# Kernel tuning notes

Measured on AMD Instinct MI355X. Metric: run time of the kernel, lower is better.

The kernel has to match this reference:

```python
import jax, jax.numpy as jnp
import numpy as np

NUM_HEADS = 12
HIDDEN = 768
HEAD = HIDDEN // NUM_HEADS
SCALE = HIDDEN ** (-0.5)  # NB: module scales by hidden_dim**-0.5, not head_size**-0.5


def setup_inputs() -> dict:
    key = jax.random.key(0)
    ks = jax.random.split(key, 8)
    B, N = 16, 512
    std = HIDDEN ** (-0.5)
    return {
        "x": jax.random.normal(ks[0], (B, N, HIDDEN), dtype=jnp.float32),
        "encoding_bias": jax.random.normal(ks[1], (B, N, N), dtype=jnp.float32),
        "Wq": jax.random.normal(ks[2], (HIDDEN, HIDDEN), dtype=jnp.float32) * std,
        "Wk": jax.random.normal(ks[3], (HIDDEN, HIDDEN), dtype=jnp.float32) * std,
        "Wv": jax.random.normal(ks[4], (HIDDEN, HIDDEN), dtype=jnp.float32) * std,
        "bv": jax.random.normal(ks[5], (HIDDEN,), dtype=jnp.float32) * 0.01,
        "Wo": jax.random.normal(ks[6], (HIDDEN, HIDDEN), dtype=jnp.float32) * std,
        "bo": jax.random.normal(ks[7], (HIDDEN,), dtype=jnp.float32) * 0.01,
    }


def reference(x, encoding_bias, Wq, Wk, Wv, bv, Wo, bo):
    B, N, _ = x.shape
    # torch nn.Linear: y = x @ W.T (+ b)
    q = (x @ Wq.T).reshape(B, N, NUM_HEADS, HEAD)
    k = (x @ Wk.T).reshape(B, N, NUM_HEADS, HEAD)
    v = (x @ Wv.T + bv).reshape(B, N, NUM_HEADS, HEAD)
    # scores: [B, H, N, N] with additive graph bias broadcast over heads
    a = jnp.einsum("bnhd,bmhd->bhnm", q, k) * SCALE + encoding_bias[:, None, :, :]
    # data-dependent pad mask: rows whose scores are identically zero
    pad_mask = jnp.all(a == 0, axis=-1)  # [B, H, N]
    a = jnp.where(pad_mask[..., None], -jnp.inf, a)
    a = jax.nn.softmax(a, axis=-1)
    a = jnp.nan_to_num(a)  # all -inf rows -> NaN -> 0
    o = jnp.einsum("bhnm,bmhd->bnhd", a, v).reshape(B, N, HIDDEN)
    # dropout is identity in eval mode
    return o @ Wo.T + bo
```

## Files before the change

kernel.cpp:

```cpp
#include <hip/hip_runtime.h>
#include <stdint.h>

typedef unsigned short u16;
typedef unsigned int u32;
typedef __bf16 bf16x8 __attribute__((ext_vector_type(8)));
typedef float f32x4 __attribute__((ext_vector_type(4)));

#define NH 12
#define HD 64
#define SEQ 512
#define BATCH 16
#define HID 768
#define SCALE_Q 0.03608439182435161f

__device__ __forceinline__ u16 f2bf(float f) {
    u32 u = __builtin_bit_cast(u32, f);
    u32 r = (u + 0x7FFFu + ((u >> 16) & 1u)) >> 16;
    return (u16)r;
}
__device__ __forceinline__ float bf2f(u16 h) {
    return __builtin_bit_cast(float, (u32)h << 16);
}

__device__ __forceinline__ void gl2lds16(const u16* g, u16* lds_base) {
    __builtin_amdgcn_global_load_lds(
        (const __attribute__((address_space(1))) u32*)g,
        (__attribute__((address_space(3))) u32*)lds_base, 16, 0, 0);
}

__global__ void cvt_kernel(const float* __restrict__ src, u16* __restrict__ dst) {
    int i = (blockIdx.x * 256 + threadIdx.x) * 4;
    float4 v = *(const float4*)(src + i);
    ushort4 o;
    o.x = f2bf(v.x); o.y = f2bf(v.y); o.z = f2bf(v.z); o.w = f2bf(v.w);
    *(ushort4*)(dst + i) = o;
}

__global__ void cvt4_kernel(const float* __restrict__ s0, const float* __restrict__ s1,
                            const float* __restrict__ s2, const float* __restrict__ s3,
                            u16* __restrict__ d0, u16* __restrict__ d1,
                            u16* __restrict__ d2, u16* __restrict__ d3) {
    int y = blockIdx.y;
    const float* s = (y == 0) ? s0 : (y == 1) ? s1 : (y == 2) ? s2 : s3;
    u16* d = (y == 0) ? d0 : (y == 1) ? d1 : (y == 2) ? d2 : d3;
    int i = (blockIdx.x * 256 + threadIdx.x) * 4;
    float4 v = *(const float4*)(s + i);
    ushort4 o;
    o.x = f2bf(v.x); o.y = f2bf(v.y); o.z = f2bf(v.z); o.w = f2bf(v.w);
    *(ushort4*)(d + i) = o;
}

__device__ __forceinline__ void gemm_mainloop(
    const u16* __restrict__ Ag, const u16* __restrict__ Bg,
    u16* As, u16* Bs, f32x4 (&acc)[4][4])
{
    const int tid = threadIdx.x;
    const int l = tid & 63, w = tid >> 6;
    const int wm = w & 1, wn = w >> 1;
    const int lr = l & 15, lg = l >> 4;

    const int c0 = tid, c1 = tid + 256;
    const int r0 = c0 >> 2, q0 = (c0 & 3) * 8;
    const int r1 = c1 >> 2, q1 = (c1 & 3) * 8;
    u16* Alds0 = As + w * 512;
    u16* Alds1 = As + 2048 + w * 512;
    u16* Blds0 = Bs + w * 512;
    u16* Blds1 = Bs + 2048 + w * 512;

    for (int k0 = 0; k0 < HID; k0 += 32) {
        __syncthreads();
        gl2lds16(Ag + (size_t)r0 * HID + k0 + q0, Alds0);
        gl2lds16(Ag + (size_t)r1 * HID + k0 + q1, Alds1);
        gl2lds16(Bg + (size_t)r0 * HID + k0 + q0, Blds0);
        gl2lds16(Bg + (size_t)r1 * HID + k0 + q1, Blds1);
        __syncthreads();

        bf16x8 af[4], bfr[4];
#pragma unroll
        for (int mi = 0; mi < 4; mi++)
            af[mi] = *(const bf16x8*)(As + (wm * 64 + mi * 16 + lr) * 32 + lg * 8);
#pragma unroll
        for (int ni = 0; ni < 4; ni++)
            bfr[ni] = *(const bf16x8*)(Bs + (wn * 64 + ni * 16 + lr) * 32 + lg * 8);
#pragma unroll
        for (int mi = 0; mi < 4; mi++)
#pragma unroll
            for (int ni = 0; ni < 4; ni++)
                acc[mi][ni] = __builtin_amdgcn_mfma_f32_16x16x32_bf16(af[mi], bfr[ni], acc[mi][ni], 0, 0, 0);
    }
}

__global__ __launch_bounds__(256, 3) void gemm_qkv(
    const u16* __restrict__ xb, const u16* __restrict__ wq,
    const u16* __restrict__ wk, const u16* __restrict__ wv,
    const float* __restrict__ bv,
    u16* __restrict__ qb, u16* __restrict__ kb, u16* __restrict__ vtb)
{
    __shared__ __align__(16) u16 As[128 * 32];
    __shared__ __align__(16) u16 Bs[128 * 32];
    const int tid = threadIdx.x;
    const int l = tid & 63, w = tid >> 6;
    const int wm = w & 1, wn = w >> 1;
    const int lr = l & 15, lg = l >> 4;
    const int mt = blockIdx.x, nt = blockIdx.y, z = blockIdx.z;

    const u16* Bw = (z == 0) ? wq : (z == 1) ? wk : wv;
    const u16* Ag = xb + (size_t)(mt * 128) * HID;
    const u16* Bg = Bw + (size_t)(nt * 128) * HID;

    f32x4 acc[4][4] = {};
    gemm_mainloop(Ag, Bg, As, Bs, acc);

    const float sc = (z == 0) ? SCALE_Q : 1.0f;
#pragma unroll
    for (int mi = 0; mi < 4; mi++) {
#pragma unroll
        for (int ni = 0; ni < 4; ni++) {
            const int jg = nt * 128 + wn * 64 + ni * 16 + lr;
            const int h = jg >> 6, d = jg & 63;
            if (z < 2) {
                u16* O = (z == 0) ? qb : kb;
#pragma unroll
                for (int r = 0; r < 4; r++) {
                    int ig = mt * 128 + wm * 64 + mi * 16 + lg * 4 + r;
                    int b = ig >> 9, n = ig & 511;
                    O[((size_t)(b * NH + h) * SEQ + n) * HD + d] = f2bf(acc[mi][ni][r] * sc);
                }
            } else {
                float bb = bv[jg];
                int i0 = mt * 128 + wm * 64 + mi * 16 + lg * 4;
                int b = i0 >> 9, m = i0 & 511;
                ushort4 pk;
                pk.x = f2bf(acc[mi][ni][0] + bb);
                pk.y = f2bf(acc[mi][ni][1] + bb);
                pk.z = f2bf(acc[mi][ni][2] + bb);
                pk.w = f2bf(acc[mi][ni][3] + bb);
                *(ushort4*)(vtb + ((size_t)(b * NH + h) * HD + d) * SEQ + m) = pk;
            }
        }
    }
}

__global__ __launch_bounds__(256, 3) void gemm_out(
    const u16* __restrict__ A, const u16* __restrict__ wo,
    const float* __restrict__ bo, float* __restrict__ Cout)
{
    __shared__ __align__(16) u16 As[128 * 32];
    __shared__ __align__(16) u16 Bs[128 * 32];
    const int tid = threadIdx.x;
    const int l = tid & 63, w = tid >> 6;
    const int wm = w & 1, wn = w >> 1;
    const int lr = l & 15, lg = l >> 4;
    const int mt = blockIdx.x, nt = blockIdx.y;

    const u16* Ag = A + (size_t)(mt * 128) * HID;
    const u16* Bg = wo + (size_t)(nt * 128) * HID;

    f32x4 acc[4][4] = {};
    gemm_mainloop(Ag, Bg, As, Bs, acc);

#pragma unroll
    for (int mi = 0; mi < 4; mi++) {
#pragma unroll
        for (int ni = 0; ni < 4; ni++) {
            const int jg = nt * 128 + wn * 64 + ni * 16 + lr;
            float bb = bo[jg];
#pragma unroll
            for (int r = 0; r < 4; r++) {
                int ig = mt * 128 + wm * 64 + mi * 16 + lg * 4 + r;
                Cout[(size_t)ig * HID + jg] = acc[mi][ni][r] + bb;
            }
        }
    }
}

#define LDA 88

__global__ __launch_bounds__(256, 4) void attn_kernel(
    const u16* __restrict__ qb, const u16* __restrict__ kb, const u16* __restrict__ vtb,
    const u16* __restrict__ ebb, u16* __restrict__ ob)
{
    __shared__ __align__(16) u16 Ks[64 * 64];
    __shared__ __align__(16) u16 Vs[64 * 64];
    __shared__ __align__(16) u16 Ps[4][16 * LDA];

    const int tid = threadIdx.x;
    const int l = tid & 63, w = tid >> 6;
    const int lr = l & 15, lg = l >> 4;
    const int qt = blockIdx.x, h = blockIdx.y, b = blockIdx.z;
    const int bh = b * NH + h;
    const int qrow0 = qt * 64 + w * 16;

    const u16* qptr = qb + ((size_t)bh * SEQ + qrow0 + lr) * HD;
    bf16x8 qf0 = *(const bf16x8*)(qptr + lg * 8);
    bf16x8 qf1 = *(const bf16x8*)(qptr + 32 + lg * 8);

    const u16* Kg = kb + (size_t)bh * SEQ * HD;
    const u16* Vg = vtb + (size_t)bh * HD * SEQ;
    const u16* Eg = ebb + ((size_t)b * SEQ + qrow0 + lg * 4) * SEQ;

    f32x4 oacc[4] = {};
    float run_m[4] = {-1e30f, -1e30f, -1e30f, -1e30f};
    float run_l[4] = {0.f, 0.f, 0.f, 0.f};
    int nzf[4] = {0, 0, 0, 0};

    const int p0 = tid, p1 = tid + 256;
    const int kr0 = p0 >> 3, kc0 = (p0 & 7) ^ (kr0 & 7);
    const int kr1 = p1 >> 3, kc1 = (p1 & 7) ^ (kr1 & 7);
    u16* Ks0 = Ks + w * 512;
    u16* Ks1 = Ks + 2048 + w * 512;
    u16* Vs0 = Vs + w * 512;
    u16* Vs1 = Vs + 2048 + w * 512;

    for (int mt0 = 0; mt0 < SEQ; mt0 += 64) {
        u16 bl[4][4];
#pragma unroll
        for (int mi = 0; mi < 4; mi++)
#pragma unroll
            for (int r = 0; r < 4; r++)
                bl[mi][r] = Eg[(size_t)r * SEQ + mt0 + mi * 16 + lr];

        __syncthreads();
        gl2lds16(Kg + (size_t)(mt0 + kr0) * HD + kc0 * 8, Ks0);
        gl2lds16(Kg + (size_t)(mt0 + kr1) * HD + kc1 * 8, Ks1);
        gl2lds16(Vg + (size_t)kr0 * SEQ + mt0 + kc0 * 8, Vs0);
        gl2lds16(Vg + (size_t)kr1 * SEQ + mt0 + kc1 * 8, Vs1);
        __syncthreads();

        float sm[4][4];
#pragma unroll
        for (int mi = 0; mi < 4; mi++) {
            const int row = mi * 16 + lr;
            bf16x8 kf0 = *(const bf16x8*)(Ks + row * 64 + ((lg ^ (row & 7)) * 8));
            bf16x8 kf1 = *(const bf16x8*)(Ks + row * 64 + (((4 + lg) ^ (row & 7)) * 8));
            f32x4 s;
#pragma unroll
            for (int r = 0; r < 4; r++) s[r] = bf2f(bl[mi][r]);
            s = __builtin_amdgcn_mfma_f32_16x16x32_bf16(qf0, kf0, s, 0, 0, 0);
            s = __builtin_amdgcn_mfma_f32_16x16x32_bf16(qf1, kf1, s, 0, 0, 0);
#pragma unroll
            for (int r = 0; r < 4; r++) {
                float sv = s[r];
                nzf[r] |= (sv != 0.0f);
                sm[mi][r] = sv;
            }
        }

        u16* Pw = Ps[w];
#pragma unroll
        for (int r = 0; r < 4; r++) {
            float tm = fmaxf(fmaxf(sm[0][r], sm[1][r]), fmaxf(sm[2][r], sm[3][r]));
            tm = fmaxf(tm, __shfl_xor(tm, 1));
            tm = fmaxf(tm, __shfl_xor(tm, 2));
            tm = fmaxf(tm, __shfl_xor(tm, 4));
            tm = fmaxf(tm, __shfl_xor(tm, 8));
            float nm = fmaxf(run_m[r], tm);
            float alpha = __expf(run_m[r] - nm);
            run_m[r] = nm;
            float ps = 0.f;
#pragma unroll
            for (int mi = 0; mi < 4; mi++) {
                float p = __expf(sm[mi][r] - nm);
                sm[mi][r] = p;
                ps += p;
            }
            ps += __shfl_xor(ps, 1);
            ps += __shfl_xor(ps, 2);
            ps += __shfl_xor(ps, 4);
            ps += __shfl_xor(ps, 8);
            run_l[r] = run_l[r] * alpha + ps;
#pragma unroll
            for (int di = 0; di < 4; di++) oacc[di][r] *= alpha;
        }
#pragma unroll
        for (int mi = 0; mi < 4; mi++)
#pragma unroll
            for (int r = 0; r < 4; r++)
                Pw[(lg * 4 + r) * LDA + mi * 16 + lr] = f2bf(sm[mi][r]);

#pragma unroll
        for (int ks = 0; ks < 2; ks++) {
            bf16x8 pf = *(const bf16x8*)(Pw + lr * LDA + ks * 32 + lg * 8);
#pragma unroll
            for (int di = 0; di < 4; di++) {
                const int row = di * 16 + lr;
                bf16x8 vf = *(const bf16x8*)(Vs + row * 64 + (((ks * 4 + lg) ^ (row & 7)) * 8));
                oacc[di] = __builtin_amdgcn_mfma_f32_16x16x32_bf16(pf, vf, oacc[di], 0, 0, 0);
            }
        }
    }

#pragma unroll
    for (int r = 0; r < 4; r++) {
        int nz = nzf[r];
        nz |= __shfl_xor(nz, 1);
        nz |= __shfl_xor(nz, 2);
        nz |= __shfl_xor(nz, 4);
        nz |= __shfl_xor(nz, 8);
        float inv = nz ? (1.0f / run_l[r]) : 0.0f;
        int n = qrow0 + lg * 4 + r;
        u16* orow = ob + ((size_t)b * SEQ + n) * HID + h * HD;
#pragma unroll
        for (int di = 0; di < 4; di++)
            orow[di * 16 + lr] = f2bf(oacc[di][r] * inv);
    }
}

extern "C" void kernel_launch(void* const* d_in, const int* in_sizes, int n_in,
                              void* d_out, int out_size, void* d_ws, size_t ws_size,
                              hipStream_t stream) {
    (void)in_sizes; (void)n_in; (void)out_size; (void)ws_size;
    const float* x  = (const float*)d_in[0];
    const float* eb = (const float*)d_in[1];
    const float* Wq = (const float*)d_in[2];
    const float* Wk = (const float*)d_in[3];
    const float* Wv = (const float*)d_in[4];
    const float* bv = (const float*)d_in[5];
    const float* Wo = (const float*)d_in[6];
    const float* bo = (const float*)d_in[7];
    float* out = (float*)d_out;

    const int NX = BATCH * SEQ * HID;
    const int NW = HID * HID;
    const int NE = BATCH * SEQ * SEQ;
    u16* ws   = (u16*)d_ws;
    u16* xb   = ws;
    u16* wqb  = xb + NX;
    u16* wkb  = wqb + NW;
    u16* wvb  = wkb + NW;
    u16* wob  = wvb + NW;
    u16* qb   = wob + NW;
    u16* kb   = qb + NX;
    u16* vtb  = kb + NX;
    u16* obuf = vtb + NX;
    u16* ebb  = obuf + NX;

    cvt_kernel<<<NX / 1024, 256, 0, stream>>>(x, xb);
    cvt_kernel<<<NE / 1024, 256, 0, stream>>>(eb, ebb);
    cvt4_kernel<<<dim3(NW / 1024, 4), 256, 0, stream>>>(Wq, Wk, Wv, Wo, wqb, wkb, wvb, wob);

    gemm_qkv<<<dim3(64, 6, 3), 256, 0, stream>>>(xb, wqb, wkb, wvb, bv, qb, kb, vtb);

    attn_kernel<<<dim3(8, NH, BATCH), 256, 0, stream>>>(qb, kb, vtb, ebb, obuf);

    gemm_out<<<dim3(64, 6), 256, 0, stream>>>(obuf, wob, bo, out);
}
```

Before: 220.3 us.

## Double-buffer GEMM and attention LDS tiles, merge conversion kernels, transpose Q store

The GEMM mainloop and the attention K/V loop now use two LDS buffers, prefetching the next tile with global-to-LDS loads while the current one is consumed, and drop one barrier per iteration. The three fp32-to-bf16 conversion launches become a single launch over a contiguous workspace. Q is written transposed with packed 4-element stores, like V, and attention gathers Q with strided scalar loads. Launch bounds change to 4 for the GEMMs and 3 for attention. The larger LDS footprint may reduce occupancy, and the strided Q reads add scattered loads.

```diff
diff --git a/kernel.cpp b/kernel.cpp
--- a/kernel.cpp
+++ b/kernel.cpp
@@ -28,31 +28,41 @@
         (__attribute__((address_space(3))) u32*)lds_base, 16, 0, 0);
 }
 
-__global__ void cvt_kernel(const float* __restrict__ src, u16* __restrict__ dst) {
-    int i = (blockIdx.x * 256 + threadIdx.x) * 4;
-    float4 v = *(const float4*)(src + i);
+#define NXB 6144
+#define NEB 4096
+#define NWB 576
+__global__ void cvt_all(const float* __restrict__ x, const float* __restrict__ eb,
+                        const float* __restrict__ w0, const float* __restrict__ w1,
+                        const float* __restrict__ w2, const float* __restrict__ w3,
+                        u16* __restrict__ dst) {
+    int b = blockIdx.x;
+    const float* s; int sb;
+    if (b < NXB) { s = x; sb = 0; }
+    else if (b < NXB + NEB) { s = eb; sb = NXB; }
+    else if (b < NXB + NEB + NWB) { s = w0; sb = NXB + NEB; }
+    else if (b < NXB + NEB + 2 * NWB) { s = w1; sb = NXB + NEB + NWB; }
+    else if (b < NXB + NEB + 3 * NWB) { s = w2; sb = NXB + NEB + 2 * NWB; }
+    else { s = w3; sb = NXB + NEB + 3 * NWB; }
+    int li = (b - sb) * 1024 + threadIdx.x * 4;
+    float4 v = *(const float4*)(s + li);
     ushort4 o;
     o.x = f2bf(v.x); o.y = f2bf(v.y); o.z = f2bf(v.z); o.w = f2bf(v.w);
-    *(ushort4*)(dst + i) = o;
-}
-
-__global__ void cvt4_kernel(const float* __restrict__ s0, const float* __restrict__ s1,
-                            const float* __restrict__ s2, const float* __restrict__ s3,
-                            u16* __restrict__ d0, u16* __restrict__ d1,
-                            u16* __restrict__ d2, u16* __restrict__ d3) {
-    int y = blockIdx.y;
-    const float* s = (y == 0) ? s0 : (y == 1) ? s1 : (y == 2) ? s2 : s3;
-    u16* d = (y == 0) ? d0 : (y == 1) ? d1 : (y == 2) ? d2 : d3;
-    int i = (blockIdx.x * 256 + threadIdx.x) * 4;
-    float4 v = *(const float4*)(s + i);
-    ushort4 o;
-    o.x = f2bf(v.x); o.y = f2bf(v.y); o.z = f2bf(v.z); o.w = f2bf(v.w);
-    *(ushort4*)(d + i) = o;
+    *(ushort4*)(dst + (size_t)b * 1024 + threadIdx.x * 4) = o;
+}
+
+__device__ __forceinline__ void stage_gemm(
+    const u16* __restrict__ Ag, const u16* __restrict__ Bg, int k0,
+    u16* As, u16* Bs, int r0, int q0, int r1, int q1, int w)
+{
+    gl2lds16(Ag + (size_t)r0 * HID + k0 + q0, As + w * 512);
+    gl2lds16(Ag + (size_t)r1 * HID + k0 + q1, As + 2048 + w * 512);
+    gl2lds16(Bg + (size_t)r0 * HID + k0 + q0, Bs + w * 512);
+    gl2lds16(Bg + (size_t)r1 * HID + k0 + q1, Bs + 2048 + w * 512);
 }
 
 __device__ __forceinline__ void gemm_mainloop(
     const u16* __restrict__ Ag, const u16* __restrict__ Bg,
-    u16* As, u16* Bs, f32x4 (&acc)[4][4])
+    u16 (*As)[128 * 32], u16 (*Bs)[128 * 32], f32x4 (&acc)[4][4])
 {
     const int tid = threadIdx.x;
     const int l = tid & 63, w = tid >> 6;
@@ -62,26 +72,22 @@
     const int c0 = tid, c1 = tid + 256;
     const int r0 = c0 >> 2, q0 = (c0 & 3) * 8;
     const int r1 = c1 >> 2, q1 = (c1 & 3) * 8;
-    u16* Alds0 = As + w * 512;
-    u16* Alds1 = As + 2048 + w * 512;
-    u16* Blds0 = Bs + w * 512;
-    u16* Blds1 = Bs + 2048 + w * 512;
-
-    for (int k0 = 0; k0 < HID; k0 += 32) {
+
+    stage_gemm(Ag, Bg, 0, As[0], Bs[0], r0, q0, r1, q1, w);
+
+    for (int i = 0; i < 24; i++) {
+        const int cur = i & 1;
         __syncthreads();
-        gl2lds16(Ag + (size_t)r0 * HID + k0 + q0, Alds0);
-        gl2lds16(Ag + (size_t)r1 * HID + k0 + q1, Alds1);
-        gl2lds16(Bg + (size_t)r0 * HID + k0 + q0, Blds0);
-        gl2lds16(Bg + (size_t)r1 * HID + k0 + q1, Blds1);
-        __syncthreads();
+        if (i < 23)
+            stage_gemm(Ag, Bg, (i + 1) * 32, As[cur ^ 1], Bs[cur ^ 1], r0, q0, r1, q1, w);
 
         bf16x8 af[4], bfr[4];
 #pragma unroll
         for (int mi = 0; mi < 4; mi++)
-            af[mi] = *(const bf16x8*)(As + (wm * 64 + mi * 16 + lr) * 32 + lg * 8);
+            af[mi] = *(const bf16x8*)(As[cur] + (wm * 64 + mi * 16 + lr) * 32 + lg * 8);
 #pragma unroll
         for (int ni = 0; ni < 4; ni++)
-            bfr[ni] = *(const bf16x8*)(Bs + (wn * 64 + ni * 16 + lr) * 32 + lg * 8);
+            bfr[ni] = *(const bf16x8*)(Bs[cur] + (wn * 64 + ni * 16 + lr) * 32 + lg * 8);
 #pragma unroll
         for (int mi = 0; mi < 4; mi++)
 #pragma unroll
@@ -90,14 +96,14 @@
     }
 }
 
-__global__ __launch_bounds__(256, 3) void gemm_qkv(
+__global__ __launch_bounds__(256, 4) void gemm_qkv(
     const u16* __restrict__ xb, const u16* __restrict__ wq,
     const u16* __restrict__ wk, const u16* __restrict__ wv,
     const float* __restrict__ bv,
-    u16* __restrict__ qb, u16* __restrict__ kb, u16* __restrict__ vtb)
-{
-    __shared__ __align__(16) u16 As[128 * 32];
-    __shared__ __align__(16) u16 Bs[128 * 32];
+    u16* __restrict__ qtb, u16* __restrict__ kb, u16* __restrict__ vtb)
+{
+    __shared__ __align__(16) u16 As[2][128 * 32];
+    __shared__ __align__(16) u16 Bs[2][128 * 32];
     const int tid = threadIdx.x;
     const int l = tid & 63, w = tid >> 6;
     const int wm = w & 1, wn = w >> 1;
@@ -118,35 +124,32 @@
         for (int ni = 0; ni < 4; ni++) {
             const int jg = nt * 128 + wn * 64 + ni * 16 + lr;
             const int h = jg >> 6, d = jg & 63;
-            if (z < 2) {
-                u16* O = (z == 0) ? qb : kb;
-#pragma unroll
-                for (int r = 0; r < 4; r++) {
-                    int ig = mt * 128 + wm * 64 + mi * 16 + lg * 4 + r;
-                    int b = ig >> 9, n = ig & 511;
-                    O[((size_t)(b * NH + h) * SEQ + n) * HD + d] = f2bf(acc[mi][ni][r] * sc);
-                }
+            const int i0 = mt * 128 + wm * 64 + mi * 16 + lg * 4;
+            const int b = i0 >> 9, n0 = i0 & 511;
+            if (z == 1) {
+#pragma unroll
+                for (int r = 0; r < 4; r++)
+                    kb[((size_t)(b * NH + h) * SEQ + n0 + r) * HD + d] = f2bf(acc[mi][ni][r]);
             } else {
-                float bb = bv[jg];
-                int i0 = mt * 128 + wm * 64 + mi * 16 + lg * 4;
-                int b = i0 >> 9, m = i0 & 511;
+                float bb = (z == 2) ? bv[jg] : 0.0f;
                 ushort4 pk;
-                pk.x = f2bf(acc[mi][ni][0] + bb);
-                pk.y = f2bf(acc[mi][ni][1] + bb);
-                pk.z = f2bf(acc[mi][ni][2] + bb);
-                pk.w = f2bf(acc[mi][ni][3] + bb);
-                *(ushort4*)(vtb + ((size_t)(b * NH + h) * HD + d) * SEQ + m) = pk;
-            }
-        }
-    }
-}
-
-__global__ __launch_bounds__(256, 3) void gemm_out(
+                pk.x = f2bf(fmaf(acc[mi][ni][0], sc, bb));
+                pk.y = f2bf(fmaf(acc[mi][ni][1], sc, bb));
+                pk.z = f2bf(fmaf(acc[mi][ni][2], sc, bb));
+                pk.w = f2bf(fmaf(acc[mi][ni][3], sc, bb));
+                u16* O = (z == 0) ? qtb : vtb;
+                *(ushort4*)(O + ((size_t)(b * NH + h) * HD + d) * SEQ + n0) = pk;
+            }
+        }
+    }
+}
+
+__global__ __launch_bounds__(256, 4) void gemm_out(
     const u16* __restrict__ A, const u16* __restrict__ wo,
     const float* __restrict__ bo, float* __restrict__ Cout)
 {
-    __shared__ __align__(16) u16 As[128 * 32];
-    __shared__ __align__(16) u16 Bs[128 * 32];
+    __shared__ __align__(16) u16 As[2][128 * 32];
+    __shared__ __align__(16) u16 Bs[2][128 * 32];
     const int tid = threadIdx.x;
     const int l = tid & 63, w = tid >> 6;
     const int wm = w & 1, wn = w >> 1;
@@ -176,12 +179,22 @@
 
 #define LDA 88
 
-__global__ __launch_bounds__(256, 4) void attn_kernel(
-    const u16* __restrict__ qb, const u16* __restrict__ kb, const u16* __restrict__ vtb,
+__device__ __forceinline__ void stage_kv(
+    const u16* __restrict__ Kg, const u16* __restrict__ Vg, int mt0,
+    u16* Ksb, u16* Vsb, int kr0, int kc0, int kr1, int kc1, int w)
+{
+    gl2lds16(Kg + (size_t)(mt0 + kr0) * HD + kc0 * 8, Ksb + w * 512);
+    gl2lds16(Kg + (size_t)(mt0 + kr1) * HD + kc1 * 8, Ksb + 2048 + w * 512);
+    gl2lds16(Vg + (size_t)kr0 * SEQ + mt0 + kc0 * 8, Vsb + w * 512);
+    gl2lds16(Vg + (size_t)kr1 * SEQ + mt0 + kc1 * 8, Vsb + 2048 + w * 512);
+}
+
+__global__ __launch_bounds__(256, 3) void attn_kernel(
+    const u16* __restrict__ qtb, const u16* __restrict__ kb, const u16* __restrict__ vtb,
     const u16* __restrict__ ebb, u16* __restrict__ ob)
 {
-    __shared__ __align__(16) u16 Ks[64 * 64];
-    __shared__ __align__(16) u16 Vs[64 * 64];
+    __shared__ __align__(16) u16 Ks[2][64 * 64];
+    __shared__ __align__(16) u16 Vs[2][64 * 64];
     __shared__ __align__(16) u16 Ps[4][16 * LDA];
 
     const int tid = threadIdx.x;
@@ -191,28 +204,34 @@
     const int bh = b * NH + h;
     const int qrow0 = qt * 64 + w * 16;
 
-    const u16* qptr = qb + ((size_t)bh * SEQ + qrow0 + lr) * HD;
-    bf16x8 qf0 = *(const bf16x8*)(qptr + lg * 8);
-    bf16x8 qf1 = *(const bf16x8*)(qptr + 32 + lg * 8);
-
     const u16* Kg = kb + (size_t)bh * SEQ * HD;
     const u16* Vg = vtb + (size_t)bh * HD * SEQ;
     const u16* Eg = ebb + ((size_t)b * SEQ + qrow0 + lg * 4) * SEQ;
+
+    const int p0 = tid, p1 = tid + 256;
+    const int kr0 = p0 >> 3, kc0 = (p0 & 7) ^ (kr0 & 7);
+    const int kr1 = p1 >> 3, kc1 = (p1 & 7) ^ (kr1 & 7);
+
+    stage_kv(Kg, Vg, 0, Ks[0], Vs[0], kr0, kc0, kr1, kc1, w);
+
+    const u16* Qg = qtb + (size_t)bh * HD * SEQ + qrow0 + lr;
+    bf16x8 qf0, qf1;
+#pragma unroll
+    for (int j = 0; j < 8; j++) {
+        qf0[j] = __builtin_bit_cast(__bf16, Qg[(size_t)(lg * 8 + j) * SEQ]);
+        qf1[j] = __builtin_bit_cast(__bf16, Qg[(size_t)(lg * 8 + j + 32) * SEQ]);
+    }
 
     f32x4 oacc[4] = {};
     float run_m[4] = {-1e30f, -1e30f, -1e30f, -1e30f};
     float run_l[4] = {0.f, 0.f, 0.f, 0.f};
     int nzf[4] = {0, 0, 0, 0};
 
-    const int p0 = tid, p1 = tid + 256;
-    const int kr0 = p0 >> 3, kc0 = (p0 & 7) ^ (kr0 & 7);
-    const int kr1 = p1 >> 3, kc1 = (p1 & 7) ^ (kr1 & 7);
-    u16* Ks0 = Ks + w * 512;
-    u16* Ks1 = Ks + 2048 + w * 512;
-    u16* Vs0 = Vs + w * 512;
-    u16* Vs1 = Vs + 2048 + w * 512;
-
-    for (int mt0 = 0; mt0 < SEQ; mt0 += 64) {
+    for (int t = 0; t < 8; t++) {
+        const int cur = t & 1;
+        const int mt0 = t * 64;
+        __syncthreads();
+
         u16 bl[4][4];
 #pragma unroll
         for (int mi = 0; mi < 4; mi++)
@@ -220,19 +239,15 @@
             for (int r = 0; r < 4; r++)
                 bl[mi][r] = Eg[(size_t)r * SEQ + mt0 + mi * 16 + lr];
 
-        __syncthreads();
-        gl2lds16(Kg + (size_t)(mt0 + kr0) * HD + kc0 * 8, Ks0);
-        gl2lds16(Kg + (size_t)(mt0 + kr1) * HD + kc1 * 8, Ks1);
-        gl2lds16(Vg + (size_t)kr0 * SEQ + mt0 + kc0 * 8, Vs0);
-        gl2lds16(Vg + (size_t)kr1 * SEQ + mt0 + kc1 * 8, Vs1);
-        __syncthreads();
+        if (t < 7)
+            stage_kv(Kg, Vg, mt0 + 64, Ks[cur ^ 1], Vs[cur ^ 1], kr0, kc0, kr1, kc1, w);
 
         float sm[4][4];
 #pragma unroll
         for (int mi = 0; mi < 4; mi++) {
             const int row = mi * 16 + lr;
-            bf16x8 kf0 = *(const bf16x8*)(Ks + row * 64 + ((lg ^ (row & 7)) * 8));
-            bf16x8 kf1 = *(const bf16x8*)(Ks + row * 64 + (((4 + lg) ^ (row & 7)) * 8));
+            bf16x8 kf0 = *(const bf16x8*)(Ks[cur] + row * 64 + ((lg ^ (row & 7)) * 8));
+            bf16x8 kf1 = *(const bf16x8*)(Ks[cur] + row * 64 + (((4 + lg) ^ (row & 7)) * 8));
             f32x4 s;
 #pragma unroll
             for (int r = 0; r < 4; r++) s[r] = bf2f(bl[mi][r]);
@@ -284,7 +299,7 @@
 #pragma unroll
             for (int di = 0; di < 4; di++) {
                 const int row = di * 16 + lr;
-                bf16x8 vf = *(const bf16x8*)(Vs + row * 64 + (((ks * 4 + lg) ^ (row & 7)) * 8));
+                bf16x8 vf = *(const bf16x8*)(Vs[cur] + row * 64 + (((ks * 4 + lg) ^ (row & 7)) * 8));
                 oacc[di] = __builtin_amdgcn_mfma_f32_16x16x32_bf16(pf, vf, oacc[di], 0, 0, 0);
             }
         }
@@ -325,23 +340,21 @@
     const int NE = BATCH * SEQ * SEQ;
     u16* ws   = (u16*)d_ws;
     u16* xb   = ws;
-    u16* wqb  = xb + NX;
+    u16* ebb  = xb + NX;
+    u16* wqb  = ebb + NE;
     u16* wkb  = wqb + NW;
     u16* wvb  = wkb + NW;
     u16* wob  = wvb + NW;
-    u16* qb   = wob + NW;
-    u16* kb   = qb + NX;
+    u16* qtb  = wob + NW;
+    u16* kb   = qtb + NX;
     u16* vtb  = kb + NX;
     u16* obuf = vtb + NX;
-    u16* ebb  = obuf + NX;
-
-    cvt_kernel<<<NX / 1024, 256, 0, stream>>>(x, xb);
-    cvt_kernel<<<NE / 1024, 256, 0, stream>>>(eb, ebb);
-    cvt4_kernel<<<dim3(NW / 1024, 4), 256, 0, stream>>>(Wq, Wk, Wv, Wo, wqb, wkb, wvb, wob);
-
-    gemm_qkv<<<dim3(64, 6, 3), 256, 0, stream>>>(xb, wqb, wkb, wvb, bv, qb, kb, vtb);
-
-    attn_kernel<<<dim3(8, NH, BATCH), 256, 0, stream>>>(qb, kb, vtb, ebb, obuf);
+
+    cvt_all<<<NXB + NEB + 4 * NWB, 256, 0, stream>>>(x, eb, Wq, Wk, Wv, Wo, ws);
+
+    gemm_qkv<<<dim3(64, 6, 3), 256, 0, stream>>>(xb, wqb, wkb, wvb, bv, qtb, kb, vtb);
+
+    attn_kernel<<<dim3(8, NH, BATCH), 256, 0, stream>>>(qtb, kb, vtb, ebb, obuf);
 
     gemm_out<<<dim3(64, 6), 256, 0, stream>>>(obuf, wob, bo, out);
 }
```

Measured after the change: 228.3 us. +3.6%, slower.
